# Optimization experiments

Hardware: AMD Instinct MI355X
Metric: run time of the kernel (lower is better)

## Reference

```python
import jax, jax.numpy as jnp
import numpy as np

B, C, H, W = 4, 192, 256, 256
WS = 8           # window_size
NH = 6           # num_heads
RS = 0.1         # residual_scale
RED = C // 16    # channel-attention reduced channels
HID = 4 * C      # ffn hidden
EPS = 1e-5


def _rel_pos_index(ws):
    coords = np.stack(np.meshgrid(np.arange(ws), np.arange(ws), indexing='ij'))  # [2,ws,ws]
    cf = coords.reshape(2, -1)
    rel = cf[:, :, None] - cf[:, None, :]            # [2,N,N]
    rel = rel.transpose(1, 2, 0).copy()
    rel[:, :, 0] += ws - 1
    rel[:, :, 1] += ws - 1
    rel[:, :, 0] *= 2 * ws - 1
    return jnp.asarray(rel.sum(-1))                  # [N,N] int

RPI = _rel_pos_index(WS)


def setup_inputs() -> dict:
    key = jax.random.key(0)
    ks = jax.random.split(key, 16)
    s = 0.02
    return {
        'x': jax.random.normal(ks[0], (B, C, H, W), jnp.float32),
        'n1_w': jnp.ones((C,), jnp.float32), 'n1_b': jnp.zeros((C,), jnp.float32),
        'n2_w': jnp.ones((C,), jnp.float32), 'n2_b': jnp.zeros((C,), jnp.float32),
        'n3_w': jnp.ones((C,), jnp.float32), 'n3_b': jnp.zeros((C,), jnp.float32),
        'ca_w1': jax.random.normal(ks[1], (RED, C), jnp.float32) * s,
        'ca_w2': jax.random.normal(ks[2], (C, RED), jnp.float32) * s,
        'qkv_w': jax.random.normal(ks[3], (3 * C, C), jnp.float32) * s,
        'proj_w': jax.random.normal(ks[4], (C, C), jnp.float32) * s,
        'proj_b': jnp.zeros((C,), jnp.float32),
        'rpb': jax.random.normal(ks[5], ((2 * WS - 1) ** 2, NH), jnp.float32) * s,
        'ffn_w1': jax.random.normal(ks[6], (HID, C), jnp.float32) * s,
        'ffn_b1': jnp.zeros((HID,), jnp.float32),
        'ffn_w2': jax.random.normal(ks[7], (C, HID), jnp.float32) * s,
        'ffn_b2': jnp.zeros((C,), jnp.float32),
    }


def _ln(x, w, b):
    m = x.mean(-1, keepdims=True)
    v = x.var(-1, keepdims=True)
    return (x - m) * jax.lax.rsqrt(v + EPS) * w + b


def reference(x, n1_w, n1_b, n2_w, n2_b, n3_w, n3_b, ca_w1, ca_w2,
              qkv_w, proj_w, proj_b, rpb, ffn_w1, ffn_b1, ffn_w2, ffn_b2):
    # --- channel attention branch ---
    res = x                                             # [B,C,H,W]
    xc = _ln(x.transpose(0, 2, 3, 1), n1_w, n1_b)       # [B,H,W,C]
    xc = xc.transpose(0, 3, 1, 2)                       # [B,C,H,W]
    y = xc.mean(axis=(2, 3))                            # [B,C] global avg pool
    y = jax.nn.relu(y @ ca_w1.T) @ ca_w2.T              # [B,C]
    y = jax.nn.sigmoid(y)[:, :, None, None]
    x = xc * y * RS + res

    # --- window attention branch ---
    res = x
    xw = _ln(x.transpose(0, 2, 3, 1), n2_w, n2_b)       # [B,H,W,C]
    nH, nW, N = H // WS, W // WS, WS * WS
    xw = xw.reshape(B, nH, WS, nW, WS, C).transpose(0, 1, 3, 2, 4, 5)
    xw = xw.reshape(B * nH * nW, N, C)                  # [Bn,N,C]

    d = C // NH
    qkv = (xw @ qkv_w.T).reshape(-1, N, 3, NH, d).transpose(2, 0, 3, 1, 4)
    q, k, v = qkv[0], qkv[1], qkv[2]                    # [Bn,NH,N,d]
    q = q * (d ** -0.5)
    attn = jnp.einsum('bhnd,bhmd->bhnm', q, k)          # [Bn,NH,N,N]
    bias = rpb[RPI.reshape(-1)].reshape(N, N, NH).transpose(2, 0, 1)
    attn = jax.nn.softmax(attn + bias[None], axis=-1)
    o = jnp.einsum('bhnm,bhmd->bhnd', attn, v)
    o = o.transpose(0, 2, 1, 3).reshape(-1, N, C)
    o = o @ proj_w.T + proj_b

    o = _ln(o, n3_w, n3_b)
    h = jax.nn.gelu(o @ ffn_w1.T + ffn_b1, approximate=False)
    o = o + (h @ ffn_w2.T + ffn_b2) * RS

    o = o.reshape(B, nH, nW, WS, WS, C).transpose(0, 1, 3, 2, 4, 5)
    o = o.reshape(B, H, W, C).transpose(0, 3, 1, 2)     # [B,C,H,W]
    return o * RS + res
```

## Files before the change

### kernel.cpp

```cpp
#include <hip/hip_runtime.h>
#include <math.h>

#define CC    192
#define WWD   256
#define HWSZ  65536
#define BB    4
#define NHD   6
#define HIDDEN 768
#define RSC   0.1f
#define EPSV  1e-5f

typedef short s8v __attribute__((ext_vector_type(8)));
typedef float f4v __attribute__((ext_vector_type(4)));
#define MFMA16(a,b,c) __builtin_amdgcn_mfma_f32_16x16x32_bf16(a,b,c,0,0,0)

__device__ __forceinline__ float b2f(unsigned short h){
  return __uint_as_float(((unsigned int)h) << 16);
}
__device__ __forceinline__ unsigned short f2b(float f){
  unsigned int u = __float_as_uint(f);
  u += 0x7FFFu + ((u >> 16) & 1u);
  return (unsigned short)(u >> 16);
}
__device__ __forceinline__ float wredsum(float v){
  #pragma unroll
  for (int off = 32; off > 0; off >>= 1) v += __shfl_xor(v, off, 64);
  return v;
}

__global__ __launch_bounds__(256) void k0_conv(
    const float* __restrict__ src, unsigned short* __restrict__ dst, int n4)
{
  int i = blockIdx.x * 256 + threadIdx.x;
  if (i < n4){
    float4 v = ((const float4*)src)[i];
    ((ushort4*)dst)[i] = make_ushort4(f2b(v.x), f2b(v.y), f2b(v.z), f2b(v.w));
  }
}

__global__ __launch_bounds__(256) void k1a_stats(
    const float* __restrict__ x, float2* __restrict__ mr)
{
  __shared__ float red[2048];
  const int pg = threadIdx.x & 63;
  const int sl = threadIdx.x >> 6;
  const int G  = blockIdx.x * 64 + pg;
  const int b  = G >> 14;
  const float* xp = x + (size_t)(b * CC) * HWSZ + ((size_t)(G & 16383) << 2);

  float sx=0.f, sy=0.f, sz=0.f, sw=0.f;
  float qx=0.f, qy=0.f, qz=0.f, qw=0.f;
  #pragma unroll 4
  for (int i = 0; i < 48; ++i){
    float4 v = *(const float4*)(xp + (size_t)(sl * 48 + i) * HWSZ);
    sx += v.x; qx += v.x * v.x;
    sy += v.y; qy += v.y * v.y;
    sz += v.z; qz += v.z * v.z;
    sw += v.w; qw += v.w * v.w;
  }
  float* rp = red + threadIdx.x * 8;
  rp[0]=sx; rp[1]=sy; rp[2]=sz; rp[3]=sw;
  rp[4]=qx; rp[5]=qy; rp[6]=qz; rp[7]=qw;
  __syncthreads();
  if (sl == 0){
    #pragma unroll
    for (int s = 1; s < 4; ++s){
      const float* o = red + (s * 64 + pg) * 8;
      sx += o[0]; sy += o[1]; sz += o[2]; sw += o[3];
      qx += o[4]; qy += o[5]; qz += o[6]; qw += o[7];
    }
    const float inv = 1.f / CC;
    float m0 = sx*inv, m1 = sy*inv, m2 = sz*inv, m3 = sw*inv;
    float4* mrv = (float4*)mr;
    mrv[G*2]   = make_float4(m0, rsqrtf(qx*inv - m0*m0 + EPSV),
                             m1, rsqrtf(qy*inv - m1*m1 + EPSV));
    mrv[G*2+1] = make_float4(m2, rsqrtf(qz*inv - m2*m2 + EPSV),
                             m3, rsqrtf(qw*inv - m3*m3 + EPSV));
  }
}

__global__ __launch_bounds__(256) void k1b_pool(
    const float* __restrict__ x, const float4* __restrict__ mrv,
    const float* __restrict__ n1w, const float* __restrict__ n1b,
    float* __restrict__ pool)
{
  int phys = blockIdx.x;
  int b = phys & 3, c = phys >> 2;
  const float4* xp = (const float4*)(x + (size_t)(b * CC + c) * HWSZ);
  const float4* mp = mrv + (size_t)b * 32768;
  float acc = 0.f;
  for (int g = threadIdx.x; g < 16384; g += 256){
    float4 v   = xp[g];
    float4 m01 = mp[2*g], m23 = mp[2*g+1];
    acc += (v.x - m01.x) * m01.y + (v.y - m01.z) * m01.w
         + (v.z - m23.x) * m23.y + (v.w - m23.z) * m23.w;
  }
  acc = wredsum(acc);
  __shared__ float r4[4];
  if ((threadIdx.x & 63) == 0) r4[threadIdx.x >> 6] = acc;
  __syncthreads();
  if (threadIdx.x == 0)
    pool[b * CC + c] = n1w[c] * (r4[0] + r4[1] + r4[2] + r4[3])
                       + 65536.f * n1b[c];
}

__global__ __launch_bounds__(256) void k2_camlp(
    const float* __restrict__ pool, const float* __restrict__ w1,
    const float* __restrict__ w2, float* __restrict__ sig)
{
  __shared__ float t[BB * 12];
  int tid = threadIdx.x;
  if (tid < BB * 12){
    int b = tid / 12, r = tid % 12;
    float a = 0.f;
    for (int c = 0; c < CC; ++c) a += pool[b * CC + c] * w1[r * CC + c];
    a *= (1.f / 65536.f);
    t[tid] = fmaxf(a, 0.f);
  }
  __syncthreads();
  for (int i = tid; i < BB * CC; i += 256){
    int b = i / CC, c = i - b * CC;
    float z = 0.f;
    #pragma unroll
    for (int r = 0; r < 12; ++r) z += t[b * 12 + r] * w2[c * 12 + r];
    sig[i] = 1.f / (1.f + __expf(-z));
  }
}

__global__ __launch_bounds__(256, 3) void k4_win(
    const float* __restrict__ x, const float2* __restrict__ mr,
    const float* __restrict__ sig,
    const float* __restrict__ n1w, const float* __restrict__ n1b,
    const float* __restrict__ n2w, const float* __restrict__ n2b,
    const float* __restrict__ n3w, const float* __restrict__ n3b,
    const unsigned short* __restrict__ qw,
    const unsigned short* __restrict__ pw,
    const float* __restrict__ projb,
    const float* __restrict__ rpb,
    const unsigned short* __restrict__ f1w,
    const float* __restrict__ fb1,
    const unsigned short* __restrict__ f2w,
    const float* __restrict__ fb2,
    float* __restrict__ out)
{
  __shared__ __align__(16) unsigned short lds[26624];
  unsigned short* Xs  = lds;
  unsigned short* Qs  = lds + 12800;
  unsigned short* Ks  = lds + 17408;
  unsigned short* VsT = lds + 22016;
  unsigned short* Hs  = lds + 12800;
  unsigned short* Ov  = lds + 12800;

  const int tid  = threadIdx.x;
  const int lane = tid & 63;
  const int wv   = tid >> 6;
  const int l15  = lane & 15;
  const int q    = lane >> 4;

  int phys = blockIdx.x;
  int blk  = ((phys & 7) << 9) | (phys >> 3);
  int b   = blk >> 10;
  int wh  = (blk >> 5) & 31;
  int ww  = blk & 31;
  size_t base = (size_t)(b * CC) * HWSZ + (size_t)(wh * 8) * WWD + ww * 8;
  int pbase = (b << 16) | ((wh * 8) << 8) | (ww * 8);

  float4 x1v[12];
  for (int kk = 0; kk < 12; ++kk){
    int idx = kk * 256 + tid;
    int c   = idx >> 4;
    int t   = idx & 15;
    int row = t >> 1, col0 = (t & 1) * 4;
    float4 xv = *(const float4*)(x + base + (size_t)c * HWSZ + row * WWD + col0);
    int px = pbase + row * 256 + col0;
    float2 m0 = mr[px], m1 = mr[px+1], m2 = mr[px+2], m3 = mr[px+3];
    float w  = n1w[c], bv = n1b[c];
    float sv = sig[b * CC + c] * RSC;
    int n0 = row * 8 + col0;
    float4 o;
    o.x = ((xv.x - m0.x) * m0.y * w + bv) * sv + xv.x;
    o.y = ((xv.y - m1.x) * m1.y * w + bv) * sv + xv.y;
    o.z = ((xv.z - m2.x) * m2.y * w + bv) * sv + xv.z;
    o.w = ((xv.w - m3.x) * m3.y * w + bv) * sv + xv.w;
    x1v[kk] = o;
    Xs[(n0    ) * 200 + c] = f2b(o.x);
    Xs[(n0 + 1) * 200 + c] = f2b(o.y);
    Xs[(n0 + 2) * 200 + c] = f2b(o.z);
    Xs[(n0 + 3) * 200 + c] = f2b(o.w);
  }
  __syncthreads();

  {
    float wa = n2w[lane], wb = n2w[lane + 64], wc = n2w[lane + 128];
    float ba = n2b[lane], bb3 = n2b[lane + 64], bc = n2b[lane + 128];
    for (int n = wv; n < 64; n += 4){
      float v0 = b2f(Xs[n * 200 + lane]);
      float v1 = b2f(Xs[n * 200 + lane + 64]);
      float v2 = b2f(Xs[n * 200 + lane + 128]);
      float s  = wredsum(v0 + v1 + v2);
      float ss = wredsum(v0 * v0 + v1 * v1 + v2 * v2);
      float mean = s * (1.f / CC);
      float rstd = rsqrtf(ss * (1.f / CC) - mean * mean + EPSV);
      Xs[n * 200 + lane]       = f2b((v0 - mean) * rstd * wa + ba);
      Xs[n * 200 + lane + 64]  = f2b((v1 - mean) * rstd * wb + bb3);
      Xs[n * 200 + lane + 128] = f2b((v2 - mean) * rstd * wc + bc);
    }
  }
  __syncthreads();

  float oreg[12][4];
  for (int pr = 0; pr < 3; ++pr){
    for (int t3 = 0; t3 < 3; ++t3){
      int t = wv * 3 + t3;
      int sel = t >> 2;
      int s = t & 3;
      const unsigned short* wrow = qw + (size_t)(sel * 192 + pr * 64 + s * 16 + l15) * 192;
      s8v Bf[6];
      #pragma unroll
      for (int k = 0; k < 6; ++k) Bf[k] = *(const s8v*)(wrow + k * 32 + q * 8);
      for (int mt = 0; mt < 4; ++mt){
        f4v acc = {0.f, 0.f, 0.f, 0.f};
        #pragma unroll
        for (int k = 0; k < 6; ++k){
          s8v Af = *(const s8v*)&Xs[(mt * 16 + l15) * 200 + k * 32 + q * 8];
          acc = MFMA16(Af, Bf[k], acc);
        }
        int row0 = mt * 16 + q * 4;
        if (sel == 0){
          #pragma unroll
          for (int r = 0; r < 4; ++r)
            Qs[(row0 + r) * 72 + s * 16 + l15] = f2b(acc[r] * 0.17677669529663689f);
        } else if (sel == 1){
          #pragma unroll
          for (int r = 0; r < 4; ++r)
            Ks[(row0 + r) * 72 + s * 16 + l15] = f2b(acc[r]);
        } else {
          #pragma unroll
          for (int r = 0; r < 4; ++r)
            VsT[(s * 16 + l15) * 72 + row0 + r] = f2b(acc[r]);
        }
      }
    }
    __syncthreads();

    float sc[2][4][4];
    {
      const s8v Aq0 = *(const s8v*)&Qs[(wv * 16 + l15) * 72 + q * 8];
      const s8v Aq1 = *(const s8v*)&Qs[(wv * 16 + l15) * 72 + 32 + q * 8];
      #pragma unroll
      for (int nt = 0; nt < 4; ++nt){
        s8v Bk0 = *(const s8v*)&Ks[(nt * 16 + l15) * 72 + q * 8];
        s8v Bk1 = *(const s8v*)&Ks[(nt * 16 + l15) * 72 + 32 + q * 8];
        f4v a0 = {0.f, 0.f, 0.f, 0.f};
        f4v a1 = {0.f, 0.f, 0.f, 0.f};
        a0 = MFMA16(Aq0, Bk0, a0);
        a1 = MFMA16(Aq1, Bk1, a1);
        #pragma unroll
        for (int r = 0; r < 4; ++r){ sc[0][nt][r] = a0[r]; sc[1][nt][r] = a1[r]; }
      }
    }
    #pragma unroll
    for (int hh = 0; hh < 2; ++hh){
      int h = pr * 2 + hh;
      #pragma unroll
      for (int r = 0; r < 4; ++r){
        int rt = wv * 16 + q * 4 + r;
        int i1 = rt >> 3, j1 = rt & 7;
        float mx = -1e30f;
        #pragma unroll
        for (int nt = 0; nt < 4; ++nt){
          int ct = nt * 16 + l15;
          int i2 = ct >> 3, j2 = ct & 7;
          sc[hh][nt][r] += rpb[((i1 - i2 + 7) * 15 + (j1 - j2 + 7)) * NHD + h];
          mx = fmaxf(mx, sc[hh][nt][r]);
        }
        #pragma unroll
        for (int m = 1; m <= 8; m <<= 1) mx = fmaxf(mx, __shfl_xor(mx, m, 64));
        float sm = 0.f;
        #pragma unroll
        for (int nt = 0; nt < 4; ++nt){
          sc[hh][nt][r] = __expf(sc[hh][nt][r] - mx);
          sm += sc[hh][nt][r];
        }
        #pragma unroll
        for (int m = 1; m <= 8; m <<= 1) sm += __shfl_xor(sm, m, 64);
        float invs = 1.f / sm;
        #pragma unroll
        for (int nt = 0; nt < 4; ++nt) sc[hh][nt][r] *= invs;
      }
    }
    #pragma unroll
    for (int hh = 0; hh < 2; ++hh){
      #pragma unroll
      for (int r = 0; r < 4; ++r)
        #pragma unroll
        for (int nt = 0; nt < 4; ++nt)
          Qs[(wv * 16 + q * 4 + r) * 72 + nt * 16 + l15] = f2b(sc[hh][nt][r]);
      #pragma unroll
      for (int vt = 0; vt < 2; ++vt){
        f4v acc = {0.f, 0.f, 0.f, 0.f};
        #pragma unroll
        for (int kst = 0; kst < 2; ++kst){
          s8v Ap = *(const s8v*)&Qs[(wv * 16 + l15) * 72 + kst * 32 + q * 8];
          s8v Bv = *(const s8v*)&VsT[(hh * 32 + vt * 16 + l15) * 72 + kst * 32 + q * 8];
          acc = MFMA16(Ap, Bv, acc);
        }
        int oi = (pr * 2 + hh) * 2 + vt;
        #pragma unroll
        for (int r = 0; r < 4; ++r) oreg[oi][r] = acc[r];
      }
    }
    __syncthreads();
  }

  #pragma unroll
  for (int oi = 0; oi < 12; ++oi){
    int h2 = oi >> 1, vt = oi & 1;
    int col = h2 * 32 + vt * 16 + l15;
    int row0 = wv * 16 + q * 4;
    #pragma unroll
    for (int r = 0; r < 4; ++r)
      Xs[(row0 + r) * 200 + col] = f2b(oreg[oi][r]);
  }
  __syncthreads();

  f4v pa[3][4];
  for (int j = 0; j < 3; ++j){
    int col = wv * 48 + j * 16 + l15;
    const unsigned short* wrow = pw + (size_t)col * 192;
    s8v Bf[6];
    #pragma unroll
    for (int k = 0; k < 6; ++k) Bf[k] = *(const s8v*)(wrow + k * 32 + q * 8);
    float bv = projb[col];
    for (int mt = 0; mt < 4; ++mt){
      f4v acc = {bv, bv, bv, bv};
      #pragma unroll
      for (int k = 0; k < 6; ++k){
        s8v Af = *(const s8v*)&Xs[(mt * 16 + l15) * 200 + k * 32 + q * 8];
        acc = MFMA16(Af, Bf[k], acc);
      }
      pa[j][mt] = acc;
    }
  }
  __syncthreads();
  #pragma unroll
  for (int j = 0; j < 3; ++j)
    for (int mt = 0; mt < 4; ++mt)
      #pragma unroll
      for (int r = 0; r < 4; ++r)
        Xs[(mt * 16 + q * 4 + r) * 200 + wv * 48 + j * 16 + l15] = f2b(pa[j][mt][r]);
  __syncthreads();

  {
    float wa = n3w[lane], wb = n3w[lane + 64], wc = n3w[lane + 128];
    float ba = n3b[lane], bb3 = n3b[lane + 64], bc = n3b[lane + 128];
    for (int n = wv; n < 64; n += 4){
      float v0 = b2f(Xs[n * 200 + lane]);
      float v1 = b2f(Xs[n * 200 + lane + 64]);
      float v2 = b2f(Xs[n * 200 + lane + 128]);
      float s  = wredsum(v0 + v1 + v2);
      float ss = wredsum(v0 * v0 + v1 * v1 + v2 * v2);
      float mean = s * (1.f / CC);
      float rstd = rsqrtf(ss * (1.f / CC) - mean * mean + EPSV);
      Xs[n * 200 + lane]       = f2b((v0 - mean) * rstd * wa + ba);
      Xs[n * 200 + lane + 64]  = f2b((v1 - mean) * rstd * wb + bb3);
      Xs[n * 200 + lane + 128] = f2b((v2 - mean) * rstd * wc + bc);
    }
  }
  __syncthreads();

  f4v facc[3][4];
  #pragma unroll
  for (int j = 0; j < 3; ++j){
    float bv = fb2[wv * 48 + j * 16 + l15];
    for (int mt = 0; mt < 4; ++mt) facc[j][mt] = (f4v){bv, bv, bv, bv};
  }
  for (int hc = 0; hc < 6; ++hc){
    for (int j = 0; j < 2; ++j){
      int hcol = hc * 128 + wv * 32 + j * 16 + l15;
      const unsigned short* wrow = f1w + (size_t)hcol * 192;
      s8v Bf[6];
      #pragma unroll
      for (int k = 0; k < 6; ++k) Bf[k] = *(const s8v*)(wrow + k * 32 + q * 8);
      float bv = fb1[hcol];
      for (int mt = 0; mt < 4; ++mt){
        f4v acc = {bv, bv, bv, bv};
        #pragma unroll
        for (int k = 0; k < 6; ++k){
          s8v Af = *(const s8v*)&Xs[(mt * 16 + l15) * 200 + k * 32 + q * 8];
          acc = MFMA16(Af, Bf[k], acc);
        }
        #pragma unroll
        for (int r = 0; r < 4; ++r){
          float g = acc[r];
          g = 0.5f * g * (1.f + erff(g * 0.70710678118654752f));
          Hs[(mt * 16 + q * 4 + r) * 136 + wv * 32 + j * 16 + l15] = f2b(g);
        }
      }
    }
    __syncthreads();
    for (int j = 0; j < 3; ++j){
      int col = wv * 48 + j * 16 + l15;
      const unsigned short* wrow = f2w + (size_t)col * HIDDEN + hc * 128;
      s8v Bf[4];
      #pragma unroll
      for (int kst = 0; kst < 4; ++kst) Bf[kst] = *(const s8v*)(wrow + kst * 32 + q * 8);
      for (int mt = 0; mt < 4; ++mt){
        f4v acc = facc[j][mt];
        #pragma unroll
        for (int kst = 0; kst < 4; ++kst){
          s8v Af = *(const s8v*)&Hs[(mt * 16 + l15) * 136 + kst * 32 + q * 8];
          acc = MFMA16(Af, Bf[kst], acc);
        }
        facc[j][mt] = acc;
      }
    }
    __syncthreads();
  }

  #pragma unroll
  for (int j = 0; j < 3; ++j)
    for (int mt = 0; mt < 4; ++mt)
      #pragma unroll
      for (int r = 0; r < 4; ++r){
        int row = mt * 16 + q * 4 + r;
        int col = wv * 48 + j * 16 + l15;
        float lv = b2f(Xs[row * 200 + col]);
        Ov[row * 196 + col] = f2b(lv + facc[j][mt][r] * RSC);
      }
  __syncthreads();

  for (int kk = 0; kk < 12; ++kk){
    int idx = kk * 256 + tid;
    int c   = idx >> 4;
    int t   = idx & 15;
    int row = t >> 1, col0 = (t & 1) * 4;
    size_t gi = base + (size_t)c * HWSZ + row * WWD + col0;
    int n0 = row * 8 + col0;
    float4 o;
    o.x = b2f(Ov[(n0    ) * 196 + c]) * RSC + x1v[kk].x;
    o.y = b2f(Ov[(n0 + 1) * 196 + c]) * RSC + x1v[kk].y;
    o.z = b2f(Ov[(n0 + 2) * 196 + c]) * RSC + x1v[kk].z;
    o.w = b2f(Ov[(n0 + 3) * 196 + c]) * RSC + x1v[kk].w;
    *(float4*)(out + gi) = o;
  }
}

extern "C" void kernel_launch(void* const* d_in, const int* in_sizes, int n_in,
                              void* d_out, int out_size, void* d_ws, size_t ws_size,
                              hipStream_t stream)
{
  const float* x    = (const float*)d_in[0];
  const float* n1w  = (const float*)d_in[1];
  const float* n1b  = (const float*)d_in[2];
  const float* n2w  = (const float*)d_in[3];
  const float* n2b  = (const float*)d_in[4];
  const float* n3w  = (const float*)d_in[5];
  const float* n3b  = (const float*)d_in[6];
  const float* caw1 = (const float*)d_in[7];
  const float* caw2 = (const float*)d_in[8];
  const float* qkvw = (const float*)d_in[9];
  const float* projw= (const float*)d_in[10];
  const float* projb= (const float*)d_in[11];
  const float* rpb  = (const float*)d_in[12];
  const float* fw1  = (const float*)d_in[13];
  const float* fb1  = (const float*)d_in[14];
  const float* fw2  = (const float*)d_in[15];
  const float* fb2  = (const float*)d_in[16];
  float* out = (float*)d_out;

  float*  pool = (float*)d_ws;
  float*  sig  = pool + 768;
  float2* mr   = (float2*)(sig + 768);
  unsigned short* qw  = (unsigned short*)((char*)d_ws + 6144 + 2097152);
  unsigned short* pwb = qw  + 110592;
  unsigned short* f1b = pwb + 36864;
  unsigned short* f2b_ = f1b + 147456;

  k0_conv<<<dim3(108), dim3(256), 0, stream>>>(qkvw, qw,  27648);
  k0_conv<<<dim3(36),  dim3(256), 0, stream>>>(projw, pwb, 9216);
  k0_conv<<<dim3(144), dim3(256), 0, stream>>>(fw1,  f1b, 36864);
  k0_conv<<<dim3(144), dim3(256), 0, stream>>>(fw2,  f2b_, 36864);

  k1a_stats<<<dim3(1024), dim3(256), 0, stream>>>(x, mr);
  k1b_pool <<<dim3(768),  dim3(256), 0, stream>>>(x, (const float4*)mr,
                                                  n1w, n1b, pool);
  k2_camlp <<<dim3(1),    dim3(256), 0, stream>>>(pool, caw1, caw2, sig);
  k4_win   <<<dim3(4096), dim3(256), 0, stream>>>(x, mr, sig, n1w, n1b,
                n2w, n2b, n3w, n3b, qw, pwb, projb, rpb, f1b, fb1, f2b_, fb2, out);
}
```

Baseline: 1.185 ms.

## Fuse stats and pooling, double-buffer FFN hidden tiles, use tanh GELU

Merges the four weight-conversion launches into one kernel. Fuses the per-pixel LayerNorm statistics and channel pooling into a single pass, using atomics into a zeroed pool buffer and moving the affine correction into the channel-attention MLP. Inside the window kernel, LayerNorms are reworked to use 16-lane reductions with register-cached weights. The FFN hidden chunks are double-buffered so each GEMM2 step overlaps with the next GEMM1 and one barrier per chunk is removed. The exact erf GELU is replaced by the tanh approximation, which changes numerics slightly, and several loops are unrolled.

Result: slower. 1.316 ms (+11.1%).

```diff
diff --git a/kernel.cpp b/kernel.cpp
--- a/kernel.cpp
+++ b/kernel.cpp
@@ -27,21 +27,36 @@
   for (int off = 32; off > 0; off >>= 1) v += __shfl_xor(v, off, 64);
   return v;
 }
-
-__global__ __launch_bounds__(256) void k0_conv(
-    const float* __restrict__ src, unsigned short* __restrict__ dst, int n4)
+__device__ __forceinline__ float gelu(float g){
+  float u = g * (0.7978845608028654f + 0.0356774081363001f * g * g);
+  float e = __expf(-2.f * fabsf(u));
+  float t = __builtin_copysignf((1.f - e) / (1.f + e), u);
+  return 0.5f * g * (1.f + t);
+}
+
+__global__ __launch_bounds__(256) void k0_all(
+    const float* __restrict__ s0, const float* __restrict__ s1,
+    const float* __restrict__ s2, const float* __restrict__ s3,
+    unsigned short* __restrict__ d0, unsigned short* __restrict__ d1,
+    unsigned short* __restrict__ d2, unsigned short* __restrict__ d3)
 {
   int i = blockIdx.x * 256 + threadIdx.x;
-  if (i < n4){
-    float4 v = ((const float4*)src)[i];
-    ((ushort4*)dst)[i] = make_ushort4(f2b(v.x), f2b(v.y), f2b(v.z), f2b(v.w));
-  }
-}
-
-__global__ __launch_bounds__(256) void k1a_stats(
-    const float* __restrict__ x, float2* __restrict__ mr)
+  const float* s; unsigned short* d; int off;
+  if (i < 27648)      { s = s0; d = d0; off = 0; }
+  else if (i < 36864) { s = s1; d = d1; off = 27648; }
+  else if (i < 73728) { s = s2; d = d2; off = 36864; }
+  else                { s = s3; d = d3; off = 73728; }
+  int j = i - off;
+  float4 v = ((const float4*)s)[j];
+  ((ushort4*)d)[j] = make_ushort4(f2b(v.x), f2b(v.y), f2b(v.z), f2b(v.w));
+}
+
+__global__ __launch_bounds__(256) void k1_fused(
+    const float* __restrict__ x, float2* __restrict__ mr,
+    float* __restrict__ pool)
 {
   __shared__ float red[2048];
+  __shared__ float mrs[512];
   const int pg = threadIdx.x & 63;
   const int sl = threadIdx.x >> 6;
   const int G  = blockIdx.x * 64 + pg;
@@ -50,7 +65,7 @@
 
   float sx=0.f, sy=0.f, sz=0.f, sw=0.f;
   float qx=0.f, qy=0.f, qz=0.f, qw=0.f;
-  #pragma unroll 4
+  #pragma unroll 8
   for (int i = 0; i < 48; ++i){
     float4 v = *(const float4*)(xp + (size_t)(sl * 48 + i) * HWSZ);
     sx += v.x; qx += v.x * v.x;
@@ -71,49 +86,43 @@
     }
     const float inv = 1.f / CC;
     float m0 = sx*inv, m1 = sy*inv, m2 = sz*inv, m3 = sw*inv;
+    float r0 = rsqrtf(qx*inv - m0*m0 + EPSV);
+    float r1 = rsqrtf(qy*inv - m1*m1 + EPSV);
+    float r2 = rsqrtf(qz*inv - m2*m2 + EPSV);
+    float r3 = rsqrtf(qw*inv - m3*m3 + EPSV);
     float4* mrv = (float4*)mr;
-    mrv[G*2]   = make_float4(m0, rsqrtf(qx*inv - m0*m0 + EPSV),
-                             m1, rsqrtf(qy*inv - m1*m1 + EPSV));
-    mrv[G*2+1] = make_float4(m2, rsqrtf(qz*inv - m2*m2 + EPSV),
-                             m3, rsqrtf(qw*inv - m3*m3 + EPSV));
-  }
-}
-
-__global__ __launch_bounds__(256) void k1b_pool(
-    const float* __restrict__ x, const float4* __restrict__ mrv,
+    mrv[G*2]   = make_float4(m0, r0, m1, r1);
+    mrv[G*2+1] = make_float4(m2, r2, m3, r3);
+    float* ms = mrs + pg * 8;
+    ms[0]=m0; ms[1]=r0; ms[2]=m1; ms[3]=r1;
+    ms[4]=m2; ms[5]=r2; ms[6]=m3; ms[7]=r3;
+  }
+  __syncthreads();
+  const float* ms = mrs + pg * 8;
+  float m0 = ms[0], r0 = ms[1], m1 = ms[2], r1 = ms[3];
+  float m2 = ms[4], r2 = ms[5], m3 = ms[6], r3 = ms[7];
+  for (int i = 0; i < 48; ++i){
+    float4 v = *(const float4*)(xp + (size_t)(sl * 48 + i) * HWSZ);
+    float t = (v.x - m0) * r0 + (v.y - m1) * r1
+            + (v.z - m2) * r2 + (v.w - m3) * r3;
+    t = wredsum(t);
+    if (pg == 0) atomicAdd(&pool[b * CC + sl * 48 + i], t);
+  }
+}
+
+__global__ __launch_bounds__(256) void k2_camlp(
+    const float* __restrict__ pool,
     const float* __restrict__ n1w, const float* __restrict__ n1b,
-    float* __restrict__ pool)
-{
-  int phys = blockIdx.x;
-  int b = phys & 3, c = phys >> 2;
-  const float4* xp = (const float4*)(x + (size_t)(b * CC + c) * HWSZ);
-  const float4* mp = mrv + (size_t)b * 32768;
-  float acc = 0.f;
-  for (int g = threadIdx.x; g < 16384; g += 256){
-    float4 v   = xp[g];
-    float4 m01 = mp[2*g], m23 = mp[2*g+1];
-    acc += (v.x - m01.x) * m01.y + (v.y - m01.z) * m01.w
-         + (v.z - m23.x) * m23.y + (v.w - m23.z) * m23.w;
-  }
-  acc = wredsum(acc);
-  __shared__ float r4[4];
-  if ((threadIdx.x & 63) == 0) r4[threadIdx.x >> 6] = acc;
-  __syncthreads();
-  if (threadIdx.x == 0)
-    pool[b * CC + c] = n1w[c] * (r4[0] + r4[1] + r4[2] + r4[3])
-                       + 65536.f * n1b[c];
-}
-
-__global__ __launch_bounds__(256) void k2_camlp(
-    const float* __restrict__ pool, const float* __restrict__ w1,
-    const float* __restrict__ w2, float* __restrict__ sig)
+    const float* __restrict__ w1, const float* __restrict__ w2,
+    float* __restrict__ sig)
 {
   __shared__ float t[BB * 12];
   int tid = threadIdx.x;
   if (tid < BB * 12){
     int b = tid / 12, r = tid % 12;
     float a = 0.f;
-    for (int c = 0; c < CC; ++c) a += pool[b * CC + c] * w1[r * CC + c];
+    for (int c = 0; c < CC; ++c)
+      a += (n1w[c] * pool[b * CC + c] + 65536.f * n1b[c]) * w1[r * CC + c];
     a *= (1.f / 65536.f);
     t[tid] = fmaxf(a, 0.f);
   }
@@ -148,7 +157,8 @@
   unsigned short* Qs  = lds + 12800;
   unsigned short* Ks  = lds + 17408;
   unsigned short* VsT = lds + 22016;
-  unsigned short* Hs  = lds + 12800;
+  unsigned short* Hs0 = lds + 12800;
+  unsigned short* Hs1 = lds + 17408;
   unsigned short* Ov  = lds + 12800;
 
   const int tid  = threadIdx.x;
@@ -166,6 +176,7 @@
   int pbase = (b << 16) | ((wh * 8) << 8) | (ww * 8);
 
   float4 x1v[12];
+  #pragma unroll
   for (int kk = 0; kk < 12; ++kk){
     int idx = kk * 256 + tid;
     int c   = idx >> 4;
@@ -173,15 +184,16 @@
     int row = t >> 1, col0 = (t & 1) * 4;
     float4 xv = *(const float4*)(x + base + (size_t)c * HWSZ + row * WWD + col0);
     int px = pbase + row * 256 + col0;
-    float2 m0 = mr[px], m1 = mr[px+1], m2 = mr[px+2], m3 = mr[px+3];
+    float4 mra = *(const float4*)(mr + px);
+    float4 mrb = *(const float4*)(mr + px + 2);
     float w  = n1w[c], bv = n1b[c];
     float sv = sig[b * CC + c] * RSC;
     int n0 = row * 8 + col0;
     float4 o;
-    o.x = ((xv.x - m0.x) * m0.y * w + bv) * sv + xv.x;
-    o.y = ((xv.y - m1.x) * m1.y * w + bv) * sv + xv.y;
-    o.z = ((xv.z - m2.x) * m2.y * w + bv) * sv + xv.z;
-    o.w = ((xv.w - m3.x) * m3.y * w + bv) * sv + xv.w;
+    o.x = ((xv.x - mra.x) * mra.y * w + bv) * sv + xv.x;
+    o.y = ((xv.y - mra.z) * mra.w * w + bv) * sv + xv.y;
+    o.z = ((xv.z - mrb.x) * mrb.y * w + bv) * sv + xv.z;
+    o.w = ((xv.w - mrb.z) * mrb.w * w + bv) * sv + xv.w;
     x1v[kk] = o;
     Xs[(n0    ) * 200 + c] = f2b(o.x);
     Xs[(n0 + 1) * 200 + c] = f2b(o.y);
@@ -191,19 +203,30 @@
   __syncthreads();
 
   {
-    float wa = n2w[lane], wb = n2w[lane + 64], wc = n2w[lane + 128];
-    float ba = n2b[lane], bb3 = n2b[lane + 64], bc = n2b[lane + 128];
-    for (int n = wv; n < 64; n += 4){
-      float v0 = b2f(Xs[n * 200 + lane]);
-      float v1 = b2f(Xs[n * 200 + lane + 64]);
-      float v2 = b2f(Xs[n * 200 + lane + 128]);
-      float s  = wredsum(v0 + v1 + v2);
-      float ss = wredsum(v0 * v0 + v1 * v1 + v2 * v2);
+    float wreg[12], breg[12];
+    #pragma unroll
+    for (int k = 0; k < 12; ++k){
+      wreg[k] = n2w[l15 + 16 * k]; breg[k] = n2b[l15 + 16 * k];
+    }
+    #pragma unroll
+    for (int it = 0; it < 4; ++it){
+      int n = it * 16 + wv * 4 + q;
+      float v[12]; float s = 0.f, ss = 0.f;
+      #pragma unroll
+      for (int k = 0; k < 12; ++k){
+        v[k] = b2f(Xs[n * 200 + l15 + 16 * k]);
+        s += v[k]; ss += v[k] * v[k];
+      }
+      #pragma unroll
+      for (int m = 1; m <= 8; m <<= 1){
+        s  += __shfl_xor(s,  m, 64);
+        ss += __shfl_xor(ss, m, 64);
+      }
       float mean = s * (1.f / CC);
       float rstd = rsqrtf(ss * (1.f / CC) - mean * mean + EPSV);
-      Xs[n * 200 + lane]       = f2b((v0 - mean) * rstd * wa + ba);
-      Xs[n * 200 + lane + 64]  = f2b((v1 - mean) * rstd * wb + bb3);
-      Xs[n * 200 + lane + 128] = f2b((v2 - mean) * rstd * wc + bc);
+      #pragma unroll
+      for (int k = 0; k < 12; ++k)
+        Xs[n * 200 + l15 + 16 * k] = f2b((v[k] - mean) * rstd * wreg[k] + breg[k]);
     }
   }
   __syncthreads();
@@ -218,6 +241,7 @@
       s8v Bf[6];
       #pragma unroll
       for (int k = 0; k < 6; ++k) Bf[k] = *(const s8v*)(wrow + k * 32 + q * 8);
+      #pragma unroll
       for (int mt = 0; mt < 4; ++mt){
         f4v acc = {0.f, 0.f, 0.f, 0.f};
         #pragma unroll
@@ -332,6 +356,7 @@
     #pragma unroll
     for (int k = 0; k < 6; ++k) Bf[k] = *(const s8v*)(wrow + k * 32 + q * 8);
     float bv = projb[col];
+    #pragma unroll
     for (int mt = 0; mt < 4; ++mt){
       f4v acc = {bv, bv, bv, bv};
       #pragma unroll
@@ -352,19 +377,30 @@
   __syncthreads();
 
   {
-    float wa = n3w[lane], wb = n3w[lane + 64], wc = n3w[lane + 128];
-    float ba = n3b[lane], bb3 = n3b[lane + 64], bc = n3b[lane + 128];
-    for (int n = wv; n < 64; n += 4){
-      float v0 = b2f(Xs[n * 200 + lane]);
-      float v1 = b2f(Xs[n * 200 + lane + 64]);
-      float v2 = b2f(Xs[n * 200 + lane + 128]);
-      float s  = wredsum(v0 + v1 + v2);
-      float ss = wredsum(v0 * v0 + v1 * v1 + v2 * v2);
+    float wreg[12], breg[12];
+    #pragma unroll
+    for (int k = 0; k < 12; ++k){
+      wreg[k] = n3w[l15 + 16 * k]; breg[k] = n3b[l15 + 16 * k];
+    }
+    #pragma unroll
+    for (int it = 0; it < 4; ++it){
+      int n = it * 16 + wv * 4 + q;
+      float v[12]; float s = 0.f, ss = 0.f;
+      #pragma unroll
+      for (int k = 0; k < 12; ++k){
+        v[k] = b2f(Xs[n * 200 + l15 + 16 * k]);
+        s += v[k]; ss += v[k] * v[k];
+      }
+      #pragma unroll
+      for (int m = 1; m <= 8; m <<= 1){
+        s  += __shfl_xor(s,  m, 64);
+        ss += __shfl_xor(ss, m, 64);
+      }
       float mean = s * (1.f / CC);
       float rstd = rsqrtf(ss * (1.f / CC) - mean * mean + EPSV);
-      Xs[n * 200 + lane]       = f2b((v0 - mean) * rstd * wa + ba);
-      Xs[n * 200 + lane + 64]  = f2b((v1 - mean) * rstd * wb + bb3);
-      Xs[n * 200 + lane + 128] = f2b((v2 - mean) * rstd * wc + bc);
+      #pragma unroll
+      for (int k = 0; k < 12; ++k)
+        Xs[n * 200 + l15 + 16 * k] = f2b((v[k] - mean) * rstd * wreg[k] + breg[k]);
     }
   }
   __syncthreads();
@@ -373,16 +409,42 @@
   #pragma unroll
   for (int j = 0; j < 3; ++j){
     float bv = fb2[wv * 48 + j * 16 + l15];
+    #pragma unroll
     for (int mt = 0; mt < 4; ++mt) facc[j][mt] = (f4v){bv, bv, bv, bv};
   }
-  for (int hc = 0; hc < 6; ++hc){
-    for (int j = 0; j < 2; ++j){
-      int hcol = hc * 128 + wv * 32 + j * 16 + l15;
+  for (int p = 0; p < 12; ++p){
+    unsigned short* Hw = (p & 1) ? Hs1 : Hs0;
+    unsigned short* Hr = (p & 1) ? Hs0 : Hs1;
+    if (p > 0){
+      s8v Ha[4][2];
+      #pragma unroll
+      for (int mt = 0; mt < 4; ++mt){
+        Ha[mt][0] = *(const s8v*)&Hr[(mt * 16 + l15) * 72 + q * 8];
+        Ha[mt][1] = *(const s8v*)&Hr[(mt * 16 + l15) * 72 + 32 + q * 8];
+      }
+      #pragma unroll
+      for (int j = 0; j < 3; ++j){
+        int col = wv * 48 + j * 16 + l15;
+        const unsigned short* wrow = f2w + (size_t)col * HIDDEN + (p - 1) * 64;
+        s8v Bf0 = *(const s8v*)(wrow + q * 8);
+        s8v Bf1 = *(const s8v*)(wrow + 32 + q * 8);
+        #pragma unroll
+        for (int mt = 0; mt < 4; ++mt){
+          f4v acc = facc[j][mt];
+          acc = MFMA16(Ha[mt][0], Bf0, acc);
+          acc = MFMA16(Ha[mt][1], Bf1, acc);
+          facc[j][mt] = acc;
+        }
+      }
+    }
+    {
+      int hcol = p * 64 + wv * 16 + l15;
       const unsigned short* wrow = f1w + (size_t)hcol * 192;
       s8v Bf[6];
       #pragma unroll
       for (int k = 0; k < 6; ++k) Bf[k] = *(const s8v*)(wrow + k * 32 + q * 8);
       float bv = fb1[hcol];
+      #pragma unroll
       for (int mt = 0; mt < 4; ++mt){
         f4v acc = {bv, bv, bv, bv};
         #pragma unroll
@@ -391,32 +453,35 @@
           acc = MFMA16(Af, Bf[k], acc);
         }
         #pragma unroll
-        for (int r = 0; r < 4; ++r){
-          float g = acc[r];
-          g = 0.5f * g * (1.f + erff(g * 0.70710678118654752f));
-          Hs[(mt * 16 + q * 4 + r) * 136 + wv * 32 + j * 16 + l15] = f2b(g);
-        }
+        for (int r = 0; r < 4; ++r)
+          Hw[(mt * 16 + q * 4 + r) * 72 + wv * 16 + l15] = f2b(gelu(acc[r]));
       }
     }
     __syncthreads();
+  }
+  {
+    s8v Ha[4][2];
+    #pragma unroll
+    for (int mt = 0; mt < 4; ++mt){
+      Ha[mt][0] = *(const s8v*)&Hs1[(mt * 16 + l15) * 72 + q * 8];
+      Ha[mt][1] = *(const s8v*)&Hs1[(mt * 16 + l15) * 72 + 32 + q * 8];
+    }
+    #pragma unroll
     for (int j = 0; j < 3; ++j){
       int col = wv * 48 + j * 16 + l15;
-      const unsigned short* wrow = f2w + (size_t)col * HIDDEN + hc * 128;
-      s8v Bf[4];
-      #pragma unroll
-      for (int kst = 0; kst < 4; ++kst) Bf[kst] = *(const s8v*)(wrow + kst * 32 + q * 8);
+      const unsigned short* wrow = f2w + (size_t)col * HIDDEN + 11 * 64;
+      s8v Bf0 = *(const s8v*)(wrow + q * 8);
+      s8v Bf1 = *(const s8v*)(wrow + 32 + q * 8);
+      #pragma unroll
       for (int mt = 0; mt < 4; ++mt){
         f4v acc = facc[j][mt];
-        #pragma unroll
-        for (int kst = 0; kst < 4; ++kst){
-          s8v Af = *(const s8v*)&Hs[(mt * 16 + l15) * 136 + kst * 32 + q * 8];
-          acc = MFMA16(Af, Bf[kst], acc);
-        }
+        acc = MFMA16(Ha[mt][0], Bf0, acc);
+        acc = MFMA16(Ha[mt][1], Bf1, acc);
         facc[j][mt] = acc;
       }
     }
-    __syncthreads();
-  }
+  }
+  __syncthreads();
 
   #pragma unroll
   for (int j = 0; j < 3; ++j)
@@ -430,6 +495,7 @@
       }
   __syncthreads();
 
+  #pragma unroll
   for (int kk = 0; kk < 12; ++kk){
     int idx = kk * 256 + tid;
     int c   = idx >> 4;
@@ -477,15 +543,11 @@
   unsigned short* f1b = pwb + 36864;
   unsigned short* f2b_ = f1b + 147456;
 
-  k0_conv<<<dim3(108), dim3(256), 0, stream>>>(qkvw, qw,  27648);
-  k0_conv<<<dim3(36),  dim3(256), 0, stream>>>(projw, pwb, 9216);
-  k0_conv<<<dim3(144), dim3(256), 0, stream>>>(fw1,  f1b, 36864);
-  k0_conv<<<dim3(144), dim3(256), 0, stream>>>(fw2,  f2b_, 36864);
-
-  k1a_stats<<<dim3(1024), dim3(256), 0, stream>>>(x, mr);
-  k1b_pool <<<dim3(768),  dim3(256), 0, stream>>>(x, (const float4*)mr,
-                                                  n1w, n1b, pool);
-  k2_camlp <<<dim3(1),    dim3(256), 0, stream>>>(pool, caw1, caw2, sig);
-  k4_win   <<<dim3(4096), dim3(256), 0, stream>>>(x, mr, sig, n1w, n1b,
+  k0_all<<<dim3(432), dim3(256), 0, stream>>>(qkvw, projw, fw1, fw2,
+                                              qw, pwb, f1b, f2b_);
+  hipMemsetAsync(pool, 0, 768 * sizeof(float), stream);
+  k1_fused<<<dim3(1024), dim3(256), 0, stream>>>(x, mr, pool);
+  k2_camlp<<<dim3(1),    dim3(256), 0, stream>>>(pool, n1w, n1b, caw1, caw2, sig);
+  k4_win  <<<dim3(4096), dim3(256), 0, stream>>>(x, mr, sig, n1w, n1b,
                 n2w, n2b, n3w, n3b, qw, pwb, projb, rpb, f1b, fb1, f2b_, fb2, out);
 }
```

## Merge weight conversion launches, unroll window-kernel loops, vectorize stats loads

Applied to the files above, without the earlier changes.

Four separate bf16 weight-conversion kernels are merged into one launch that picks source and destination by index range, removing three launch overheads. The window kernel gets explicit unroll pragmas on its MFMA tile loops and load/store loops, and reads the per-pixel mean/rstd pairs as two float4 loads instead of four float2 loads. The occupancy hint moves from a launch_bounds min-blocks value to amdgpu_waves_per_eu(3,3), which can change register allocation. Extra unrolling may raise register pressure and risk spills at the fixed occupancy target.

New measurement: 1.172 ms. No clear change (-1.1%).

```diff
diff --git a/kernel.cpp b/kernel.cpp
--- a/kernel.cpp
+++ b/kernel.cpp
@@ -28,14 +28,21 @@
   return v;
 }
 
-__global__ __launch_bounds__(256) void k0_conv(
-    const float* __restrict__ src, unsigned short* __restrict__ dst, int n4)
+__global__ __launch_bounds__(256) void k0_all(
+    const float* __restrict__ s0, const float* __restrict__ s1,
+    const float* __restrict__ s2, const float* __restrict__ s3,
+    unsigned short* __restrict__ d0, unsigned short* __restrict__ d1,
+    unsigned short* __restrict__ d2, unsigned short* __restrict__ d3)
 {
   int i = blockIdx.x * 256 + threadIdx.x;
-  if (i < n4){
-    float4 v = ((const float4*)src)[i];
-    ((ushort4*)dst)[i] = make_ushort4(f2b(v.x), f2b(v.y), f2b(v.z), f2b(v.w));
-  }
+  const float* s; unsigned short* d; int off;
+  if (i < 27648)      { s = s0; d = d0; off = 0; }
+  else if (i < 36864) { s = s1; d = d1; off = 27648; }
+  else if (i < 73728) { s = s2; d = d2; off = 36864; }
+  else                { s = s3; d = d3; off = 73728; }
+  int j = i - off;
+  float4 v = ((const float4*)s)[j];
+  ((ushort4*)d)[j] = make_ushort4(f2b(v.x), f2b(v.y), f2b(v.z), f2b(v.w));
 }
 
 __global__ __launch_bounds__(256) void k1a_stats(
@@ -127,7 +134,9 @@
   }
 }
 
-__global__ __launch_bounds__(256, 3) void k4_win(
+__global__ void __launch_bounds__(256)
+__attribute__((amdgpu_waves_per_eu(3, 3)))
+k4_win(
     const float* __restrict__ x, const float2* __restrict__ mr,
     const float* __restrict__ sig,
     const float* __restrict__ n1w, const float* __restrict__ n1b,
@@ -166,6 +175,7 @@
   int pbase = (b << 16) | ((wh * 8) << 8) | (ww * 8);
 
   float4 x1v[12];
+  #pragma unroll
   for (int kk = 0; kk < 12; ++kk){
     int idx = kk * 256 + tid;
     int c   = idx >> 4;
@@ -173,15 +183,16 @@
     int row = t >> 1, col0 = (t & 1) * 4;
     float4 xv = *(const float4*)(x + base + (size_t)c * HWSZ + row * WWD + col0);
     int px = pbase + row * 256 + col0;
-    float2 m0 = mr[px], m1 = mr[px+1], m2 = mr[px+2], m3 = mr[px+3];
+    float4 mra = *(const float4*)(mr + px);
+    float4 mrb = *(const float4*)(mr + px + 2);
     float w  = n1w[c], bv = n1b[c];
     float sv = sig[b * CC + c] * RSC;
     int n0 = row * 8 + col0;
     float4 o;
-    o.x = ((xv.x - m0.x) * m0.y * w + bv) * sv + xv.x;
-    o.y = ((xv.y - m1.x) * m1.y * w + bv) * sv + xv.y;
-    o.z = ((xv.z - m2.x) * m2.y * w + bv) * sv + xv.z;
-    o.w = ((xv.w - m3.x) * m3.y * w + bv) * sv + xv.w;
+    o.x = ((xv.x - mra.x) * mra.y * w + bv) * sv + xv.x;
+    o.y = ((xv.y - mra.z) * mra.w * w + bv) * sv + xv.y;
+    o.z = ((xv.z - mrb.x) * mrb.y * w + bv) * sv + xv.z;
+    o.w = ((xv.w - mrb.z) * mrb.w * w + bv) * sv + xv.w;
     x1v[kk] = o;
     Xs[(n0    ) * 200 + c] = f2b(o.x);
     Xs[(n0 + 1) * 200 + c] = f2b(o.y);
@@ -218,6 +229,7 @@
       s8v Bf[6];
       #pragma unroll
       for (int k = 0; k < 6; ++k) Bf[k] = *(const s8v*)(wrow + k * 32 + q * 8);
+      #pragma unroll
       for (int mt = 0; mt < 4; ++mt){
         f4v acc = {0.f, 0.f, 0.f, 0.f};
         #pragma unroll
@@ -332,6 +344,7 @@
     #pragma unroll
     for (int k = 0; k < 6; ++k) Bf[k] = *(const s8v*)(wrow + k * 32 + q * 8);
     float bv = projb[col];
+    #pragma unroll
     for (int mt = 0; mt < 4; ++mt){
       f4v acc = {bv, bv, bv, bv};
       #pragma unroll
@@ -373,6 +386,7 @@
   #pragma unroll
   for (int j = 0; j < 3; ++j){
     float bv = fb2[wv * 48 + j * 16 + l15];
+    #pragma unroll
     for (int mt = 0; mt < 4; ++mt) facc[j][mt] = (f4v){bv, bv, bv, bv};
   }
   for (int hc = 0; hc < 6; ++hc){
@@ -383,6 +397,7 @@
       #pragma unroll
       for (int k = 0; k < 6; ++k) Bf[k] = *(const s8v*)(wrow + k * 32 + q * 8);
       float bv = fb1[hcol];
+      #pragma unroll
       for (int mt = 0; mt < 4; ++mt){
         f4v acc = {bv, bv, bv, bv};
         #pragma unroll
@@ -405,6 +420,7 @@
       s8v Bf[4];
       #pragma unroll
       for (int kst = 0; kst < 4; ++kst) Bf[kst] = *(const s8v*)(wrow + kst * 32 + q * 8);
+      #pragma unroll
       for (int mt = 0; mt < 4; ++mt){
         f4v acc = facc[j][mt];
         #pragma unroll
@@ -430,6 +446,7 @@
       }
   __syncthreads();
 
+  #pragma unroll
   for (int kk = 0; kk < 12; ++kk){
     int idx = kk * 256 + tid;
     int c   = idx >> 4;
@@ -477,11 +494,8 @@
   unsigned short* f1b = pwb + 36864;
   unsigned short* f2b_ = f1b + 147456;
 
-  k0_conv<<<dim3(108), dim3(256), 0, stream>>>(qkvw, qw,  27648);
-  k0_conv<<<dim3(36),  dim3(256), 0, stream>>>(projw, pwb, 9216);
-  k0_conv<<<dim3(144), dim3(256), 0, stream>>>(fw1,  f1b, 36864);
-  k0_conv<<<dim3(144), dim3(256), 0, stream>>>(fw2,  f2b_, 36864);
-
+  k0_all<<<dim3(432), dim3(256), 0, stream>>>(qkvw, projw, fw1, fw2,
+                                              qw, pwb, f1b, f2b_);
   k1a_stats<<<dim3(1024), dim3(256), 0, stream>>>(x, mr);
   k1b_pool <<<dim3(768),  dim3(256), 0, stream>>>(x, (const float4*)mr,
                                                   n1w, n1b, pool);
```
